# Kernel optimization log

Measured on AMD Instinct MI355X. Metric: run time of the kernel, lower is better.

The kernel has to match this reference:

```python
import jax, jax.numpy as jnp
import numpy as np

B, S, H, D, K = 262144, 120, 256, 64, 64  # batch, state_dim, vae_hidden_dim, latent_dim, n_codes


def _lin(k, i, o):
    return jax.random.normal(k, (i, o), jnp.float32) / np.sqrt(i).astype(np.float32)


def setup_inputs() -> dict:
    key = jax.random.key(0)
    ks = jax.random.split(key, 9)
    return {
        "inputs": jax.random.normal(ks[0], (B, S), jnp.float32),
        "enc_w1": _lin(ks[1], S, H), "enc_b1": jnp.zeros((H,), jnp.float32),
        "enc_w2": _lin(ks[2], H, H), "enc_b2": jnp.zeros((H,), jnp.float32),
        "enc_w3": _lin(ks[3], H, D), "enc_b3": jnp.zeros((D,), jnp.float32),
        "codebook": jax.random.uniform(ks[4], (K, D), jnp.float32),  # NearestEmbed weight (rand init)
        "fc3_w": _lin(ks[5], D, H), "fc3_b": jnp.zeros((H,), jnp.float32),
        "fc4_w": _lin(ks[6], H, H), "fc4_b": jnp.zeros((H,), jnp.float32),
        "fc5_w": _lin(ks[7], H, S), "fc5_b": jnp.zeros((S,), jnp.float32),
    }


def _nearest(z, codebook):
    # squared L2 distance via |z|^2 - 2 z.C^T + |c|^2; fused GEMM form
    d = ((z * z).sum(-1, keepdims=True)
         - 2.0 * (z @ codebook.T)
         + (codebook * codebook).sum(-1))  # [B, K]
    idx = jnp.argmin(d, axis=-1)  # [B]
    return codebook[idx], idx


def reference(inputs, enc_w1, enc_b1, enc_w2, enc_b2, enc_w3, enc_b3,
              codebook, fc3_w, fc3_b, fc4_w, fc4_b, fc5_w, fc5_b):
    # encode
    h = jax.nn.relu(inputs @ enc_w1 + enc_b1)
    h = jax.nn.relu(h @ enc_w2 + enc_b2)
    z_e = h @ enc_w3 + enc_b3  # [B, D]
    # emb(z_e, weight_sg=True): straight-through to input, codebook detached
    q, argmin = _nearest(z_e, jax.lax.stop_gradient(codebook))
    z_q = z_e + jax.lax.stop_gradient(q - z_e)
    # emb(z_e.detach()): grads flow only to codebook
    emb, _ = _nearest(jax.lax.stop_gradient(z_e), codebook)
    # decode (recon_type=1)
    r = jax.nn.relu(z_q @ fc3_w + fc3_b)
    r = jax.nn.relu(r @ fc4_w + fc4_b)
    s_hat = r @ fc5_w + fc5_b  # [B, S]
    return s_hat, z_e, emb, argmin
```

## Files before the change

### kernel.cpp

```cpp
#include <hip/hip_runtime.h>


#define B_TOTAL 262144
#define THR 0.02f

typedef float  f32x4 __attribute__((ext_vector_type(4)));
typedef short  s16x8 __attribute__((ext_vector_type(8)));

#define ZB ((size_t)B_TOTAL * 120)
#define EB ((size_t)B_TOTAL * 184)
#define AB ((size_t)B_TOTAL * 248)

#define WS_STAB   0
#define WS_CBT    30720
#define WS_CNORM  47104
#define WS_COUNT  47360
#define WS_LIST   47424
#define WS_PKW1   1096064
#define WS_PKW2   1227136
#define WS_PKE3   1489280
#define WS_PKCB   1554816

static __device__ __forceinline__ unsigned short f2bf(float x) {
    unsigned int u = __float_as_uint(x);
    return (unsigned short)((u + 0x7fffu + ((u >> 16) & 1u)) >> 16);
}
static __device__ __forceinline__ void splitbf(float a, unsigned short& h, unsigned short& s) {
    unsigned hb = __float_as_uint(a) & 0xffff0000u;
    h = (unsigned short)(hb >> 16);
    s = f2bf(a - __uint_as_float(hb));
}
static __device__ __forceinline__ float sqnc(float v) {
    float s = v * v;
    asm volatile("" : "+v"(s));
    return s;
}
static __device__ __forceinline__ float np_sumsq64(const float* a) {
    float r8[8];
#pragma unroll
    for (int j = 0; j < 8; ++j) r8[j] = sqnc(a[j]);
#pragma unroll
    for (int i = 8; i < 64; i += 8)
#pragma unroll
        for (int j = 0; j < 8; ++j) r8[j] += sqnc(a[i + j]);
    return ((r8[0] + r8[1]) + (r8[2] + r8[3])) + ((r8[4] + r8[5]) + (r8[6] + r8[7]));
}

static __device__ __forceinline__ int swz(int row, int col) {
    return row * 256 + ((((col >> 3) ^ (row & 7))) << 3) + (col & 7);
}

__global__ __launch_bounds__(256)
void vq_prep(const float* __restrict__ cb,
             const float* __restrict__ dw3, const float* __restrict__ db3,
             const float* __restrict__ dw4, const float* __restrict__ db4,
             const float* __restrict__ dw5, const float* __restrict__ db5,
             float* __restrict__ s_tab, float* __restrict__ cbT, float* __restrict__ cnorm)
{
    __shared__ float c_row[64];
    __shared__ float u1[256];
    __shared__ float u2[256];
    const int k = blockIdx.x;
    const int t = threadIdx.x;

    if (t < 64) c_row[t] = cb[k * 64 + t];
    __syncthreads();
    {
        float s = 0.f;
        for (int f = 0; f < 64; ++f) s = fmaf(c_row[f], dw3[f * 256 + t], s);
        u1[t] = fmaxf(s + db3[t], 0.f);
    }
    if (t < 64) cbT[t * 64 + k] = c_row[t];
    if (t == 0) cnorm[k] = np_sumsq64(&cb[k * 64]);
    __syncthreads();
    {
        float s = 0.f;
        for (int f = 0; f < 256; ++f) s = fmaf(u1[f], dw4[f * 256 + t], s);
        u2[t] = fmaxf(s + db4[t], 0.f);
    }
    __syncthreads();
    if (t < 120) {
        float o = 0.f;
        for (int f = 0; f < 256; ++f) o = fmaf(u2[f], dw5[f * 120 + t], o);
        s_tab[k * 120 + t] = o + db5[t];
    }
}

__global__ __launch_bounds__(512)
void vq_pack(const float* __restrict__ w1, const float* __restrict__ w2,
             const float* __restrict__ ew3, const float* __restrict__ cbT,
             unsigned short* __restrict__ pw1, unsigned short* __restrict__ pw2,
             unsigned short* __restrict__ pe3, unsigned short* __restrict__ pcb,
             int* __restrict__ flag_count)
{
    const int t = threadIdx.x;
    int f = blockIdx.x;
    if (f == 0 && t == 0) *flag_count = 0;

    const float* src; unsigned short* dst;
    int KSN, nt, ks, srcK, ld;
    if (f < 64)       { src = w1;  dst = pw1; KSN = 4; nt = f >> 2;  ks = f & 3; srcK = 120; ld = 256; }
    else if (f < 192) { f -= 64;  src = w2;  dst = pw2; KSN = 8; nt = f >> 3; ks = f & 7; srcK = 256; ld = 256; }
    else if (f < 224) { f -= 192; src = ew3; dst = pe3; KSN = 8; nt = f >> 3; ks = f & 7; srcK = 256; ld = 64; }
    else              { f -= 224; src = cbT; dst = pcb; KSN = 2; nt = f >> 1; ks = f & 1; srcK = 64;  ld = 64; }

    const int lane = t >> 3, j = t & 7;
    const int k = ks * 32 + (lane >> 4) * 8 + j;
    const int n = nt * 16 + (lane & 15);
    float a = (k < srcK) ? src[k * ld + n] : 0.f;
    unsigned short h, l;
    splitbf(a, h, l);
    const int base = (nt * KSN + ks) * 2 * 512;
    dst[base + t] = h;
    dst[base + 512 + t] = l;
}

__global__ __launch_bounds__(512, 4)
void vq_fast(const float* __restrict__ x,
             const float* __restrict__ b1, const float* __restrict__ b2,
             const float* __restrict__ eb3, const float* __restrict__ cb,
             const float* __restrict__ s_tab, const float* __restrict__ cnorm,
             const unsigned short* __restrict__ pw1, const unsigned short* __restrict__ pw2,
             const unsigned short* __restrict__ pe3, const unsigned short* __restrict__ pcb,
             int* __restrict__ flag_count, int* __restrict__ flag_list,
             float* __restrict__ out)
{
    __shared__ __align__(16) unsigned char smem[65536];
    unsigned short* ph = (unsigned short*)smem;
    unsigned short* pl = (unsigned short*)(smem + 32768);
    unsigned short* zh = (unsigned short*)smem;
    unsigned short* zl = (unsigned short*)(smem + 9216);
    float*          dm = (float*)(smem + 18432);
    int*          idxs = (int*)(smem + 35840);

    const int t = threadIdx.x;
    const int w = t >> 6, l = t & 63;
    const int lr = l & 15;
    const int grow0 = blockIdx.x * 64;

    {
        const float* xb = x + (size_t)grow0 * 120;
        unsigned* ph32 = (unsigned*)ph;
        unsigned* pl32 = (unsigned*)pl;
#pragma unroll
        for (int i = 0; i < 8; ++i) {
            int p = t + 512 * i;
            if (p < 3840) {
                int row = p / 60, c2 = p - row * 60;
                float2 v = *(const float2*)&xb[row * 120 + c2 * 2];
                unsigned short h0, l0, h1, l1;
                splitbf(v.x, h0, l0); splitbf(v.y, h1, l1);
                int o32 = row * 128 + ((((c2 >> 2) ^ (row & 7))) << 2) + (c2 & 3);
                ph32[o32] = (unsigned)h0 | ((unsigned)h1 << 16);
                pl32[o32] = (unsigned)l0 | ((unsigned)l1 << 16);
            }
        }
        if (t < 256) {
            int row = t >> 2, c2 = 60 + (t & 3);
            int o32 = row * 128 + ((((c2 >> 2) ^ (row & 7))) << 2) + (c2 & 3);
            ph32[o32] = 0u;
            pl32[o32] = 0u;
        }
    }
    __syncthreads();

    const int wrow = w >> 2, wcol = w & 3;
    const int rbase = wrow * 32, cbase = wcol * 64;

    {
        f32x4 acc[2][4];
#pragma unroll
        for (int a = 0; a < 2; ++a)
#pragma unroll
            for (int b = 0; b < 4; ++b) acc[a][b] = (f32x4)0.f;

#pragma unroll
        for (int ks = 0; ks < 4; ++ks) {
            const int kb = ks * 32 + (l >> 4) * 8;
            s16x8 ah[2], al[2];
#pragma unroll
            for (int rt = 0; rt < 2; ++rt) {
                const int ro = swz(rbase + rt * 16 + lr, kb);
                ah[rt] = *(const s16x8*)&ph[ro];
                al[rt] = *(const s16x8*)&pl[ro];
            }
#pragma unroll
            for (int ct = 0; ct < 4; ++ct) {
                const unsigned short* pb = pw1 + ((wcol * 4 + ct) * 4 + ks) * 2 * 512 + l * 8;
                s16x8 bh = *(const s16x8*)pb;
                s16x8 bl = *(const s16x8*)(pb + 512);
                __builtin_amdgcn_s_setprio(1);
#pragma unroll
                for (int rt = 0; rt < 2; ++rt) {
                    acc[rt][ct] = __builtin_amdgcn_mfma_f32_16x16x32_bf16(ah[rt], bh, acc[rt][ct], 0, 0, 0);
                    acc[rt][ct] = __builtin_amdgcn_mfma_f32_16x16x32_bf16(ah[rt], bl, acc[rt][ct], 0, 0, 0);
                    acc[rt][ct] = __builtin_amdgcn_mfma_f32_16x16x32_bf16(al[rt], bh, acc[rt][ct], 0, 0, 0);
                }
                __builtin_amdgcn_s_setprio(0);
            }
        }
        __syncthreads();
#pragma unroll
        for (int ct = 0; ct < 4; ++ct) {
            const int col = cbase + ct * 16 + lr;
            const float bb = b1[col];
#pragma unroll
            for (int rt = 0; rt < 2; ++rt)
#pragma unroll
                for (int r = 0; r < 4; ++r) {
                    float v = fmaxf(acc[rt][ct][r] + bb, 0.f);
                    unsigned short h, s;
                    splitbf(v, h, s);
                    const int row = rbase + rt * 16 + (l >> 4) * 4 + r;
                    const int o = swz(row, col);
                    ph[o] = h;
                    pl[o] = s;
                }
        }
    }
    __syncthreads();

    {
        f32x4 acc[2][4];
#pragma unroll
        for (int a = 0; a < 2; ++a)
#pragma unroll
            for (int b = 0; b < 4; ++b) acc[a][b] = (f32x4)0.f;

#pragma unroll
        for (int ks = 0; ks < 8; ++ks) {
            const int kb = ks * 32 + (l >> 4) * 8;
            s16x8 ah[2], al[2];
#pragma unroll
            for (int rt = 0; rt < 2; ++rt) {
                const int ro = swz(rbase + rt * 16 + lr, kb);
                ah[rt] = *(const s16x8*)&ph[ro];
                al[rt] = *(const s16x8*)&pl[ro];
            }
#pragma unroll
            for (int ct = 0; ct < 4; ++ct) {
                const unsigned short* pb = pw2 + ((wcol * 4 + ct) * 8 + ks) * 2 * 512 + l * 8;
                s16x8 bh = *(const s16x8*)pb;
                s16x8 bl = *(const s16x8*)(pb + 512);
                __builtin_amdgcn_s_setprio(1);
#pragma unroll
                for (int rt = 0; rt < 2; ++rt) {
                    acc[rt][ct] = __builtin_amdgcn_mfma_f32_16x16x32_bf16(ah[rt], bh, acc[rt][ct], 0, 0, 0);
                    acc[rt][ct] = __builtin_amdgcn_mfma_f32_16x16x32_bf16(ah[rt], bl, acc[rt][ct], 0, 0, 0);
                    acc[rt][ct] = __builtin_amdgcn_mfma_f32_16x16x32_bf16(al[rt], bh, acc[rt][ct], 0, 0, 0);
                }
                __builtin_amdgcn_s_setprio(0);
            }
        }
        __syncthreads();
#pragma unroll
        for (int ct = 0; ct < 4; ++ct) {
            const int col = cbase + ct * 16 + lr;
            const float bb = b2[col];
#pragma unroll
            for (int rt = 0; rt < 2; ++rt)
#pragma unroll
                for (int r = 0; r < 4; ++r) {
                    float v = fmaxf(acc[rt][ct][r] + bb, 0.f);
                    unsigned short h, s;
                    splitbf(v, h, s);
                    const int row = rbase + rt * 16 + (l >> 4) * 4 + r;
                    const int o = swz(row, col);
                    ph[o] = h;
                    pl[o] = s;
                }
        }
    }
    __syncthreads();

    const int r3 = (w & 3) * 16;
    const int ch = w >> 2;
    {
        f32x4 a3[2];
#pragma unroll
        for (int b = 0; b < 2; ++b) a3[b] = (f32x4)0.f;

#pragma unroll
        for (int ks = 0; ks < 8; ++ks) {
            const int kb = ks * 32 + (l >> 4) * 8;
            const int ro = swz(r3 + lr, kb);
            s16x8 ah = *(const s16x8*)&ph[ro];
            s16x8 al = *(const s16x8*)&pl[ro];
#pragma unroll
            for (int ct = 0; ct < 2; ++ct) {
                const unsigned short* pb = pe3 + ((ch * 2 + ct) * 8 + ks) * 2 * 512 + l * 8;
                s16x8 bh = *(const s16x8*)pb;
                s16x8 bl = *(const s16x8*)(pb + 512);
                __builtin_amdgcn_s_setprio(1);
                a3[ct] = __builtin_amdgcn_mfma_f32_16x16x32_bf16(ah, bh, a3[ct], 0, 0, 0);
                a3[ct] = __builtin_amdgcn_mfma_f32_16x16x32_bf16(ah, bl, a3[ct], 0, 0, 0);
                a3[ct] = __builtin_amdgcn_mfma_f32_16x16x32_bf16(al, bh, a3[ct], 0, 0, 0);
                __builtin_amdgcn_s_setprio(0);
            }
        }
        __syncthreads();
#pragma unroll
        for (int ct = 0; ct < 2; ++ct) {
            const int col = ch * 32 + ct * 16 + lr;
            const float eb = eb3[col];
#pragma unroll
            for (int r = 0; r < 4; ++r) {
                const int row = r3 + (l >> 4) * 4 + r;
                float z = a3[ct][r] + eb;
                out[ZB + (size_t)(grow0 + row) * 64 + col] = z;
                unsigned short h, s;
                splitbf(z, h, s);
                zh[row * 72 + col] = h;
                zl[row * 72 + col] = s;
            }
        }
    }
    __syncthreads();

    {
        f32x4 a4[2];
#pragma unroll
        for (int b = 0; b < 2; ++b) a4[b] = (f32x4)0.f;
#pragma unroll
        for (int ks = 0; ks < 2; ++ks) {
            const int kb = ks * 32 + (l >> 4) * 8;
            const int ro = (r3 + lr) * 72 + kb;
            s16x8 ah = *(const s16x8*)&zh[ro];
            s16x8 al = *(const s16x8*)&zl[ro];
#pragma unroll
            for (int ct = 0; ct < 2; ++ct) {
                const unsigned short* pb = pcb + ((ch * 2 + ct) * 2 + ks) * 2 * 512 + l * 8;
                s16x8 bh = *(const s16x8*)pb;
                s16x8 bl = *(const s16x8*)(pb + 512);
                __builtin_amdgcn_s_setprio(1);
                a4[ct] = __builtin_amdgcn_mfma_f32_16x16x32_bf16(ah, bh, a4[ct], 0, 0, 0);
                a4[ct] = __builtin_amdgcn_mfma_f32_16x16x32_bf16(ah, bl, a4[ct], 0, 0, 0);
                a4[ct] = __builtin_amdgcn_mfma_f32_16x16x32_bf16(al, bh, a4[ct], 0, 0, 0);
                __builtin_amdgcn_s_setprio(0);
            }
        }
#pragma unroll
        for (int ct = 0; ct < 2; ++ct) {
            const int col = ch * 32 + ct * 16 + lr;
            const float cn = cnorm[col];
#pragma unroll
            for (int r = 0; r < 4; ++r) {
                const int row = r3 + (l >> 4) * 4 + r;
                dm[row * 68 + col] = cn - 2.f * a4[ct][r];
            }
        }
    }
    __syncthreads();

    if (t < 64) {
        const float* dr = dm + t * 68;
        float best = dr[0], sec = 3.4e38f;
        int bi = 0;
        for (int j = 1; j < 64; ++j) {
            float v = dr[j];
            if (v < best) { sec = best; best = v; bi = j; }
            else if (v < sec) sec = v;
        }
        idxs[t] = bi;
        out[AB + grow0 + t] = (float)bi;
        if (sec - best < THR) {
            int p = atomicAdd(flag_count, 1);
            if (p < B_TOTAL) flag_list[p] = grow0 + t;
        }
    }
    __syncthreads();

#pragma unroll
    for (int i = 0; i < 8; ++i) {
        int p = t + 512 * i;
        int row = p >> 6, c = p & 63;
        out[EB + (size_t)blockIdx.x * 4096 + p] = cb[idxs[row] * 64 + c];
    }
#pragma unroll
    for (int i = 0; i < 15; ++i) {
        int p = t + 512 * i;
        int row = p / 120, c = p - row * 120;
        out[(size_t)blockIdx.x * 7680 + p] = s_tab[idxs[row] * 120 + c];
    }
}

__global__ __launch_bounds__(256)
void vq_exact(const float* __restrict__ x,
              const float* __restrict__ w1, const float* __restrict__ b1,
              const float* __restrict__ w2, const float* __restrict__ b2,
              const float* __restrict__ ew3, const float* __restrict__ eb3,
              const float* __restrict__ cb,
              const float* __restrict__ s_tab,
              const float* __restrict__ cbT, const float* __restrict__ cnorm,
              const int* __restrict__ flag_count, const int* __restrict__ flag_list,
              float* __restrict__ out)
{
    __shared__ float act[256 * 18];
    __shared__ float zrm[16 * 68];
    __shared__ float dmr[16 * 68];
    __shared__ float A_lds[16];
    __shared__ int   idxs[16];
    __shared__ int   rl[16];

    const int t = threadIdx.x;
    int count = *flag_count;
    if (count > B_TOTAL) count = B_TOTAL;

    const int tx = t & 31;
    const int ty = t >> 5;
    const int r0 = ty * 2;
    const int c0 = tx * 8;
    const int c0d = tx * 2;

    for (int base = blockIdx.x * 16; base < count; base += 1024 * 16) {
        if (t < 16) {
            int li = base + t;
            rl[t] = flag_list[li < count ? li : count - 1];
        }
        __syncthreads();

        for (int i = 0; i < 8; ++i) {
            int p = t + 256 * i;
            if (p < 1920) {
                int r = p / 120;
                int c = p - r * 120;
                act[c * 18 + r] = x[(size_t)rl[r] * 120 + c];
            }
        }
        __syncthreads();

        {
            float acc[2][8];
#pragma unroll
            for (int i = 0; i < 2; ++i)
#pragma unroll
                for (int c = 0; c < 8; ++c) acc[i][c] = 0.f;
#pragma unroll 2
            for (int k = 0; k < 120; ++k) {
                const float2 av = *(const float2*)&act[k * 18 + r0];
                const float4 wv0 = *(const float4*)&w1[k * 256 + c0];
                const float4 wv1 = *(const float4*)&w1[k * 256 + c0 + 4];
                const float a[2] = {av.x, av.y};
                const float wv[8] = {wv0.x, wv0.y, wv0.z, wv0.w, wv1.x, wv1.y, wv1.z, wv1.w};
#pragma unroll
                for (int i = 0; i < 2; ++i)
#pragma unroll
                    for (int c = 0; c < 8; ++c) acc[i][c] = fmaf(a[i], wv[c], acc[i][c]);
            }
            __syncthreads();
            const float4 bv0 = *(const float4*)&b1[c0];
            const float4 bv1 = *(const float4*)&b1[c0 + 4];
            const float bb[8] = {bv0.x, bv0.y, bv0.z, bv0.w, bv1.x, bv1.y, bv1.z, bv1.w};
#pragma unroll
            for (int c = 0; c < 8; ++c)
#pragma unroll
                for (int i = 0; i < 2; ++i)
                    act[(c0 + c) * 18 + r0 + i] = fmaxf(acc[i][c] + bb[c], 0.f);
        }
        __syncthreads();

        {
            float acc[2][8];
#pragma unroll
            for (int i = 0; i < 2; ++i)
#pragma unroll
                for (int c = 0; c < 8; ++c) acc[i][c] = 0.f;
#pragma unroll 2
            for (int k = 0; k < 256; ++k) {
                const float2 av = *(const float2*)&act[k * 18 + r0];
                const float4 wv0 = *(const float4*)&w2[k * 256 + c0];
                const float4 wv1 = *(const float4*)&w2[k * 256 + c0 + 4];
                const float a[2] = {av.x, av.y};
                const float wv[8] = {wv0.x, wv0.y, wv0.z, wv0.w, wv1.x, wv1.y, wv1.z, wv1.w};
#pragma unroll
                for (int i = 0; i < 2; ++i)
#pragma unroll
                    for (int c = 0; c < 8; ++c) acc[i][c] = fmaf(a[i], wv[c], acc[i][c]);
            }
            __syncthreads();
            const float4 bv0 = *(const float4*)&b2[c0];
            const float4 bv1 = *(const float4*)&b2[c0 + 4];
            const float bb[8] = {bv0.x, bv0.y, bv0.z, bv0.w, bv1.x, bv1.y, bv1.z, bv1.w};
#pragma unroll
            for (int c = 0; c < 8; ++c)
#pragma unroll
                for (int i = 0; i < 2; ++i)
                    act[(c0 + c) * 18 + r0 + i] = fmaxf(acc[i][c] + bb[c], 0.f);
        }
        __syncthreads();

        {
            float acc2[2][2];
#pragma unroll
            for (int i = 0; i < 2; ++i) { acc2[i][0] = 0.f; acc2[i][1] = 0.f; }
#pragma unroll 2
            for (int k = 0; k < 256; ++k) {
                const float2 av = *(const float2*)&act[k * 18 + r0];
                const float2 wv = *(const float2*)&ew3[k * 64 + c0d];
#pragma unroll
                for (int i = 0; i < 2; ++i) {
                    float a = (i == 0) ? av.x : av.y;
                    acc2[i][0] = fmaf(a, wv.x, acc2[i][0]);
                    acc2[i][1] = fmaf(a, wv.y, acc2[i][1]);
                }
            }
            __syncthreads();
            const float2 bv = *(const float2*)&eb3[c0d];
#pragma unroll
            for (int i = 0; i < 2; ++i) {
                float z0 = acc2[i][0] + bv.x;
                float z1 = acc2[i][1] + bv.y;
                act[(c0d + 0) * 18 + r0 + i] = z0;
                act[(c0d + 1) * 18 + r0 + i] = z1;
                zrm[(r0 + i) * 68 + c0d]     = z0;
                zrm[(r0 + i) * 68 + c0d + 1] = z1;
            }
        }
        __syncthreads();

        if (t < 16) A_lds[t] = np_sumsq64(&zrm[t * 68]);
        __syncthreads();

        {
            float acc3[2][2];
#pragma unroll
            for (int i = 0; i < 2; ++i) { acc3[i][0] = 0.f; acc3[i][1] = 0.f; }
#pragma unroll 2
            for (int k = 0; k < 64; ++k) {
                const float2 av = *(const float2*)&act[k * 18 + r0];
                const float2 wv = *(const float2*)&cbT[k * 64 + c0d];
#pragma unroll
                for (int i = 0; i < 2; ++i) {
                    float a = (i == 0) ? av.x : av.y;
                    acc3[i][0] = fmaf(a, wv.x, acc3[i][0]);
                    acc3[i][1] = fmaf(a, wv.y, acc3[i][1]);
                }
            }
            const float cn0 = cnorm[c0d], cn1 = cnorm[c0d + 1];
#pragma unroll
            for (int i = 0; i < 2; ++i) {
                float g0 = 2.0f * acc3[i][0];  asm volatile("" : "+v"(g0));
                float g1 = 2.0f * acc3[i][1];  asm volatile("" : "+v"(g1));
                const float Ar = A_lds[r0 + i];
                dmr[(r0 + i) * 68 + c0d]     = (Ar - g0) + cn0;
                dmr[(r0 + i) * 68 + c0d + 1] = (Ar - g1) + cn1;
            }
        }
        __syncthreads();

        if (t < 16) {
            const float* dr = &dmr[t * 68];
            float best = dr[0];
            int bi = 0;
            for (int c = 1; c < 64; ++c) {
                float v = dr[c];
                if (v < best) { best = v; bi = c; }
            }
            idxs[t] = bi;
            out[AB + rl[t]] = (float)bi;
        }
        __syncthreads();

        {
            const int r = t >> 4, q = t & 15;
            *(float4*)(out + ZB + (size_t)rl[r] * 64 + q * 4) = *(const float4*)&zrm[r * 68 + q * 4];
        }
        {
            const int r = t >> 4, q = t & 15;
            *(float4*)(out + EB + (size_t)rl[r] * 64 + q * 4) = *(const float4*)(cb + idxs[r] * 64 + q * 4);
        }
        for (int i = 0; i < 8; ++i) {
            int p = t + 256 * i;
            if (p < 1920) {
                int r = p / 120;
                int c = p - r * 120;
                out[(size_t)rl[r] * 120 + c] = s_tab[idxs[r] * 120 + c];
            }
        }
        __syncthreads();
    }
}

extern "C" void kernel_launch(void* const* d_in, const int* in_sizes, int n_in,
                              void* d_out, int out_size, void* d_ws, size_t ws_size,
                              hipStream_t stream)
{
    const float* x   = (const float*)d_in[0];
    const float* w1  = (const float*)d_in[1];
    const float* b1  = (const float*)d_in[2];
    const float* w2  = (const float*)d_in[3];
    const float* b2  = (const float*)d_in[4];
    const float* ew3 = (const float*)d_in[5];
    const float* eb3 = (const float*)d_in[6];
    const float* cb  = (const float*)d_in[7];
    const float* dw3 = (const float*)d_in[8];
    const float* db3 = (const float*)d_in[9];
    const float* dw4 = (const float*)d_in[10];
    const float* db4 = (const float*)d_in[11];
    const float* dw5 = (const float*)d_in[12];
    const float* db5 = (const float*)d_in[13];

    float* out = (float*)d_out;
    char* ws = (char*)d_ws;
    float* s_tab = (float*)(ws + WS_STAB);
    float* cbT   = (float*)(ws + WS_CBT);
    float* cnorm = (float*)(ws + WS_CNORM);
    int*   fcnt  = (int*)(ws + WS_COUNT);
    int*   flist = (int*)(ws + WS_LIST);
    unsigned short* pw1 = (unsigned short*)(ws + WS_PKW1);
    unsigned short* pw2 = (unsigned short*)(ws + WS_PKW2);
    unsigned short* pe3 = (unsigned short*)(ws + WS_PKE3);
    unsigned short* pcb = (unsigned short*)(ws + WS_PKCB);

    vq_prep<<<64, 256, 0, stream>>>(cb, dw3, db3, dw4, db4, dw5, db5,
                                    s_tab, cbT, cnorm);
    vq_pack<<<232, 512, 0, stream>>>(w1, w2, ew3, cbT, pw1, pw2, pe3, pcb, fcnt);
    vq_fast<<<B_TOTAL / 64, 512, 0, stream>>>(x, b1, b2, eb3, cb, s_tab, cnorm,
                                              pw1, pw2, pe3, pcb, fcnt, flist, out);
    vq_exact<<<1024, 256, 0, stream>>>(x, w1, b1, w2, b2, ew3, eb3, cb,
                                       s_tab, cbT, cnorm, fcnt, flist, out);
}
```

Measured before the change: 492.9 us.

## Truncate bf16 split, batch B-fragment loads, widen exact-path grid and unroll

Replaces the round-to-nearest low-part bf16 split with plain truncation, and packs the input split with fewer shifts. MFMA loops now load B fragments for two column tiles before issuing the MFMAs, and the setprio region moves outside the inner loop. The fallback exact kernel launches twice as many blocks and unrolls its fp32 k-loops more deeply. Truncating the low part slightly lowers the accuracy of the three-product bf16 emulation, which could change which rows get flagged for the exact path.

```diff
diff --git a/kernel.cpp b/kernel.cpp
--- a/kernel.cpp
+++ b/kernel.cpp
@@ -29,6 +29,12 @@
     unsigned hb = __float_as_uint(a) & 0xffff0000u;
     h = (unsigned short)(hb >> 16);
     s = f2bf(a - __uint_as_float(hb));
+}
+static __device__ __forceinline__ void splitbf_t(float a, unsigned short& h, unsigned short& s) {
+    unsigned u = __float_as_uint(a);
+    h = (unsigned short)(u >> 16);
+    float d = a - __uint_as_float(u & 0xffff0000u);
+    s = (unsigned short)(__float_as_uint(d) >> 16);
 }
 static __device__ __forceinline__ float sqnc(float v) {
     float s = v * v;
@@ -148,11 +154,15 @@
             if (p < 3840) {
                 int row = p / 60, c2 = p - row * 60;
                 float2 v = *(const float2*)&xb[row * 120 + c2 * 2];
-                unsigned short h0, l0, h1, l1;
-                splitbf(v.x, h0, l0); splitbf(v.y, h1, l1);
+                unsigned u0 = __float_as_uint(v.x);
+                unsigned u1 = __float_as_uint(v.y);
+                unsigned h0u = u0 & 0xffff0000u;
+                unsigned h1u = u1 & 0xffff0000u;
+                float d0 = v.x - __uint_as_float(h0u);
+                float d1 = v.y - __uint_as_float(h1u);
                 int o32 = row * 128 + ((((c2 >> 2) ^ (row & 7))) << 2) + (c2 & 3);
-                ph32[o32] = (unsigned)h0 | ((unsigned)h1 << 16);
-                pl32[o32] = (unsigned)l0 | ((unsigned)l1 << 16);
+                ph32[o32] = (u0 >> 16) | h1u;
+                pl32[o32] = (__float_as_uint(d0) >> 16) | (__float_as_uint(d1) & 0xffff0000u);
             }
         }
         if (t < 256) {
@@ -185,16 +195,24 @@
                 al[rt] = *(const s16x8*)&pl[ro];
             }
 #pragma unroll
-            for (int ct = 0; ct < 4; ++ct) {
-                const unsigned short* pb = pw1 + ((wcol * 4 + ct) * 4 + ks) * 2 * 512 + l * 8;
-                s16x8 bh = *(const s16x8*)pb;
-                s16x8 bl = *(const s16x8*)(pb + 512);
+            for (int cp = 0; cp < 2; ++cp) {
+                s16x8 bh[2], bl[2];
+#pragma unroll
+                for (int j = 0; j < 2; ++j) {
+                    const unsigned short* pb = pw1 + ((wcol * 4 + cp * 2 + j) * 4 + ks) * 2 * 512 + l * 8;
+                    bh[j] = *(const s16x8*)pb;
+                    bl[j] = *(const s16x8*)(pb + 512);
+                }
                 __builtin_amdgcn_s_setprio(1);
 #pragma unroll
-                for (int rt = 0; rt < 2; ++rt) {
-                    acc[rt][ct] = __builtin_amdgcn_mfma_f32_16x16x32_bf16(ah[rt], bh, acc[rt][ct], 0, 0, 0);
-                    acc[rt][ct] = __builtin_amdgcn_mfma_f32_16x16x32_bf16(ah[rt], bl, acc[rt][ct], 0, 0, 0);
-                    acc[rt][ct] = __builtin_amdgcn_mfma_f32_16x16x32_bf16(al[rt], bh, acc[rt][ct], 0, 0, 0);
+                for (int j = 0; j < 2; ++j) {
+                    const int ct = cp * 2 + j;
+#pragma unroll
+                    for (int rt = 0; rt < 2; ++rt) {
+                        acc[rt][ct] = __builtin_amdgcn_mfma_f32_16x16x32_bf16(ah[rt], bh[j], acc[rt][ct], 0, 0, 0);
+                        acc[rt][ct] = __builtin_amdgcn_mfma_f32_16x16x32_bf16(ah[rt], bl[j], acc[rt][ct], 0, 0, 0);
+                        acc[rt][ct] = __builtin_amdgcn_mfma_f32_16x16x32_bf16(al[rt], bh[j], acc[rt][ct], 0, 0, 0);
+                    }
                 }
                 __builtin_amdgcn_s_setprio(0);
             }
@@ -210,7 +228,7 @@
                 for (int r = 0; r < 4; ++r) {
                     float v = fmaxf(acc[rt][ct][r] + bb, 0.f);
                     unsigned short h, s;
-                    splitbf(v, h, s);
+                    splitbf_t(v, h, s);
                     const int row = rbase + rt * 16 + (l >> 4) * 4 + r;
                     const int o = swz(row, col);
                     ph[o] = h;
@@ -238,16 +256,24 @@
                 al[rt] = *(const s16x8*)&pl[ro];
             }
 #pragma unroll
-            for (int ct = 0; ct < 4; ++ct) {
-                const unsigned short* pb = pw2 + ((wcol * 4 + ct) * 8 + ks) * 2 * 512 + l * 8;
-                s16x8 bh = *(const s16x8*)pb;
-                s16x8 bl = *(const s16x8*)(pb + 512);
+            for (int cp = 0; cp < 2; ++cp) {
+                s16x8 bh[2], bl[2];
+#pragma unroll
+                for (int j = 0; j < 2; ++j) {
+                    const unsigned short* pb = pw2 + ((wcol * 4 + cp * 2 + j) * 8 + ks) * 2 * 512 + l * 8;
+                    bh[j] = *(const s16x8*)pb;
+                    bl[j] = *(const s16x8*)(pb + 512);
+                }
                 __builtin_amdgcn_s_setprio(1);
 #pragma unroll
-                for (int rt = 0; rt < 2; ++rt) {
-                    acc[rt][ct] = __builtin_amdgcn_mfma_f32_16x16x32_bf16(ah[rt], bh, acc[rt][ct], 0, 0, 0);
-                    acc[rt][ct] = __builtin_amdgcn_mfma_f32_16x16x32_bf16(ah[rt], bl, acc[rt][ct], 0, 0, 0);
-                    acc[rt][ct] = __builtin_amdgcn_mfma_f32_16x16x32_bf16(al[rt], bh, acc[rt][ct], 0, 0, 0);
+                for (int j = 0; j < 2; ++j) {
+                    const int ct = cp * 2 + j;
+#pragma unroll
+                    for (int rt = 0; rt < 2; ++rt) {
+                        acc[rt][ct] = __builtin_amdgcn_mfma_f32_16x16x32_bf16(ah[rt], bh[j], acc[rt][ct], 0, 0, 0);
+                        acc[rt][ct] = __builtin_amdgcn_mfma_f32_16x16x32_bf16(ah[rt], bl[j], acc[rt][ct], 0, 0, 0);
+                        acc[rt][ct] = __builtin_amdgcn_mfma_f32_16x16x32_bf16(al[rt], bh[j], acc[rt][ct], 0, 0, 0);
+                    }
                 }
                 __builtin_amdgcn_s_setprio(0);
             }
@@ -263,7 +289,7 @@
                 for (int r = 0; r < 4; ++r) {
                     float v = fmaxf(acc[rt][ct][r] + bb, 0.f);
                     unsigned short h, s;
-                    splitbf(v, h, s);
+                    splitbf_t(v, h, s);
                     const int row = rbase + rt * 16 + (l >> 4) * 4 + r;
                     const int o = swz(row, col);
                     ph[o] = h;
@@ -286,17 +312,21 @@
             const int ro = swz(r3 + lr, kb);
             s16x8 ah = *(const s16x8*)&ph[ro];
             s16x8 al = *(const s16x8*)&pl[ro];
+            s16x8 bh[2], bl[2];
 #pragma unroll
             for (int ct = 0; ct < 2; ++ct) {
                 const unsigned short* pb = pe3 + ((ch * 2 + ct) * 8 + ks) * 2 * 512 + l * 8;
-                s16x8 bh = *(const s16x8*)pb;
-                s16x8 bl = *(const s16x8*)(pb + 512);
-                __builtin_amdgcn_s_setprio(1);
-                a3[ct] = __builtin_amdgcn_mfma_f32_16x16x32_bf16(ah, bh, a3[ct], 0, 0, 0);
-                a3[ct] = __builtin_amdgcn_mfma_f32_16x16x32_bf16(ah, bl, a3[ct], 0, 0, 0);
-                a3[ct] = __builtin_amdgcn_mfma_f32_16x16x32_bf16(al, bh, a3[ct], 0, 0, 0);
-                __builtin_amdgcn_s_setprio(0);
-            }
+                bh[ct] = *(const s16x8*)pb;
+                bl[ct] = *(const s16x8*)(pb + 512);
+            }
+            __builtin_amdgcn_s_setprio(1);
+#pragma unroll
+            for (int ct = 0; ct < 2; ++ct) {
+                a3[ct] = __builtin_amdgcn_mfma_f32_16x16x32_bf16(ah, bh[ct], a3[ct], 0, 0, 0);
+                a3[ct] = __builtin_amdgcn_mfma_f32_16x16x32_bf16(ah, bl[ct], a3[ct], 0, 0, 0);
+                a3[ct] = __builtin_amdgcn_mfma_f32_16x16x32_bf16(al, bh[ct], a3[ct], 0, 0, 0);
+            }
+            __builtin_amdgcn_s_setprio(0);
         }
         __syncthreads();
 #pragma unroll
@@ -309,7 +339,7 @@
                 float z = a3[ct][r] + eb;
                 out[ZB + (size_t)(grow0 + row) * 64 + col] = z;
                 unsigned short h, s;
-                splitbf(z, h, s);
+                splitbf_t(z, h, s);
                 zh[row * 72 + col] = h;
                 zl[row * 72 + col] = s;
             }
@@ -327,17 +357,21 @@
             const int ro = (r3 + lr) * 72 + kb;
             s16x8 ah = *(const s16x8*)&zh[ro];
             s16x8 al = *(const s16x8*)&zl[ro];
+            s16x8 bh[2], bl[2];
 #pragma unroll
             for (int ct = 0; ct < 2; ++ct) {
                 const unsigned short* pb = pcb + ((ch * 2 + ct) * 2 + ks) * 2 * 512 + l * 8;
-                s16x8 bh = *(const s16x8*)pb;
-                s16x8 bl = *(const s16x8*)(pb + 512);
-                __builtin_amdgcn_s_setprio(1);
-                a4[ct] = __builtin_amdgcn_mfma_f32_16x16x32_bf16(ah, bh, a4[ct], 0, 0, 0);
-                a4[ct] = __builtin_amdgcn_mfma_f32_16x16x32_bf16(ah, bl, a4[ct], 0, 0, 0);
-                a4[ct] = __builtin_amdgcn_mfma_f32_16x16x32_bf16(al, bh, a4[ct], 0, 0, 0);
-                __builtin_amdgcn_s_setprio(0);
-            }
+                bh[ct] = *(const s16x8*)pb;
+                bl[ct] = *(const s16x8*)(pb + 512);
+            }
+            __builtin_amdgcn_s_setprio(1);
+#pragma unroll
+            for (int ct = 0; ct < 2; ++ct) {
+                a4[ct] = __builtin_amdgcn_mfma_f32_16x16x32_bf16(ah, bh[ct], a4[ct], 0, 0, 0);
+                a4[ct] = __builtin_amdgcn_mfma_f32_16x16x32_bf16(ah, bl[ct], a4[ct], 0, 0, 0);
+                a4[ct] = __builtin_amdgcn_mfma_f32_16x16x32_bf16(al, bh[ct], a4[ct], 0, 0, 0);
+            }
+            __builtin_amdgcn_s_setprio(0);
         }
 #pragma unroll
         for (int ct = 0; ct < 2; ++ct) {
@@ -412,7 +446,7 @@
     const int c0 = tx * 8;
     const int c0d = tx * 2;
 
-    for (int base = blockIdx.x * 16; base < count; base += 1024 * 16) {
+    for (int base = blockIdx.x * 16; base < count; base += 2048 * 16) {
         if (t < 16) {
             int li = base + t;
             rl[t] = flag_list[li < count ? li : count - 1];
@@ -435,7 +469,7 @@
             for (int i = 0; i < 2; ++i)
 #pragma unroll
                 for (int c = 0; c < 8; ++c) acc[i][c] = 0.f;
-#pragma unroll 2
+#pragma unroll 8
             for (int k = 0; k < 120; ++k) {
                 const float2 av = *(const float2*)&act[k * 18 + r0];
                 const float4 wv0 = *(const float4*)&w1[k * 256 + c0];
@@ -465,7 +499,7 @@
             for (int i = 0; i < 2; ++i)
 #pragma unroll
                 for (int c = 0; c < 8; ++c) acc[i][c] = 0.f;
-#pragma unroll 2
+#pragma unroll 8
             for (int k = 0; k < 256; ++k) {
                 const float2 av = *(const float2*)&act[k * 18 + r0];
                 const float4 wv0 = *(const float4*)&w2[k * 256 + c0];
@@ -493,7 +527,7 @@
             float acc2[2][2];
 #pragma unroll
             for (int i = 0; i < 2; ++i) { acc2[i][0] = 0.f; acc2[i][1] = 0.f; }
-#pragma unroll 2
+#pragma unroll 8
             for (int k = 0; k < 256; ++k) {
                 const float2 av = *(const float2*)&act[k * 18 + r0];
                 const float2 wv = *(const float2*)&ew3[k * 64 + c0d];
@@ -525,7 +559,7 @@
             float acc3[2][2];
 #pragma unroll
             for (int i = 0; i < 2; ++i) { acc3[i][0] = 0.f; acc3[i][1] = 0.f; }
-#pragma unroll 2
+#pragma unroll 8
             for (int k = 0; k < 64; ++k) {
                 const float2 av = *(const float2*)&act[k * 18 + r0];
                 const float2 wv = *(const float2*)&cbT[k * 64 + c0d];
@@ -617,6 +651,6 @@
     vq_pack<<<232, 512, 0, stream>>>(w1, w2, ew3, cbT, pw1, pw2, pe3, pcb, fcnt);
     vq_fast<<<B_TOTAL / 64, 512, 0, stream>>>(x, b1, b2, eb3, cb, s_tab, cnorm,
                                               pw1, pw2, pe3, pcb, fcnt, flist, out);
-    vq_exact<<<1024, 256, 0, stream>>>(x, w1, b1, w2, b2, ew3, eb3, cb,
+    vq_exact<<<2048, 256, 0, stream>>>(x, w1, b1, w2, b2, ew3, eb3, cb,
                                        s_tab, cbT, cnorm, fcnt, flist, out);
 }
```

Result: no change. 489.1 us (-0.8%).
